# Kernel optimization log

Measured on AMD Instinct MI355X. Metric: run time of the kernel, lower is better.

The kernel has to match this reference:

```python
import jax, jax.numpy as jnp
import numpy as np
from jax import lax


def setup_inputs() -> dict:
    key = jax.random.key(0)
    k1, k2, k3 = jax.random.split(key, 3)
    B, T, D, K = 64, 512, 1024, 32
    x = jax.random.normal(k1, (B, T, D), dtype=jnp.float32)
    W = jax.random.normal(k2, (D, K), dtype=jnp.float32) * (1.0 / np.sqrt(D))
    U = jax.random.normal(k3, (K, K), dtype=jnp.float32) * 0.1
    b = jnp.zeros((K,), dtype=jnp.float32)
    return {"x": x, "W": W, "U": U, "b": b}


def _crf_marginals(x, W, U, b):
    # Emission (input) energies: linear activation of x @ W + b -> [B, T, K]
    e = jnp.einsum('btd,dk->btk', x, W) + b
    e_t = jnp.swapaxes(e, 0, 1)  # [T, B, K]

    # Forward recursion: alpha_t = logsumexp_prev(alpha_{t-1} + U) + e_t
    def fwd_step(alpha, et):
        a = jax.nn.logsumexp(alpha[:, :, None] + U[None, :, :], axis=1) + et
        return a, a

    alpha0 = e_t[0]
    _, alphas = lax.scan(fwd_step, alpha0, e_t[1:])
    alpha = jnp.concatenate([alpha0[None], alphas], axis=0)  # [T, B, K]

    # Backward recursion: beta_t = logsumexp_next(U + e_{t+1} + beta_{t+1})
    def bwd_step(beta, et_next):
        nb = jax.nn.logsumexp(U[None, :, :] + (et_next + beta)[:, None, :], axis=2)
        return nb, nb

    betaT = jnp.zeros_like(alpha0)
    _, betas = lax.scan(bwd_step, betaT, e_t[1:], reverse=True)
    beta = jnp.concatenate([betas, betaT[None]], axis=0)  # [T, B, K]

    # Marginal probability of each tag at each timestep
    marg = jax.nn.softmax(alpha + beta, axis=-1)  # [T, B, K]
    return jnp.swapaxes(marg, 0, 1)  # [B, T, K]


def reference(x, W, U, b):
    return _crf_marginals(x, W, U, b)
```

## Files before the change

kernel.cpp:

```cpp
#include <hip/hip_runtime.h>
#include <stdint.h>

#define TT 512
#define BB 64
#define DD 1024
#define KK 32

typedef __attribute__((ext_vector_type(8))) short short8v;
typedef __attribute__((ext_vector_type(4))) float f4v;

__device__ __forceinline__ float rfl(float v) {
  return __int_as_float(__builtin_amdgcn_readfirstlane(__float_as_int(v)));
}

__device__ __forceinline__ void cvt2(float f0, float f1,
                                     unsigned& h, unsigned& lo) {
  unsigned u0 = __float_as_uint(f0), u1 = __float_as_uint(f1);
  h = (u1 & 0xFFFF0000u) | (u0 >> 16);
  float r0 = f0 - __uint_as_float(u0 & 0xFFFF0000u);
  float r1 = f1 - __uint_as_float(u1 & 0xFFFF0000u);
  lo = (__float_as_uint(r1) & 0xFFFF0000u) | (__float_as_uint(r0) >> 16);
}

__global__ __launch_bounds__(256) void wconv_kernel(
    const float* __restrict__ W, uint4* __restrict__ Wf) {
  const int t = blockIdx.x * 256 + threadIdx.x;
  const int l = t & 63;
  const int kt = (t >> 6) & 1;
  const int c = t >> 7;
  const int d0 = c * 32 + (l >> 4) * 8;
  const int k = kt * 16 + (l & 15);
  unsigned h[4], q[4];
#pragma unroll
  for (int j = 0; j < 4; ++j) {
    float f0 = W[(size_t)(d0 + 2 * j) * KK + k];
    float f1 = W[(size_t)(d0 + 2 * j + 1) * KK + k];
    cvt2(f0, f1, h[j], q[j]);
  }
  Wf[(size_t)(c * 4 + kt * 2 + 0) * 64 + l] = make_uint4(h[0], h[1], h[2], h[3]);
  Wf[(size_t)(c * 4 + kt * 2 + 1) * 64 + l] = make_uint4(q[0], q[1], q[2], q[3]);
}

__global__ __launch_bounds__(256, 4) void emit_kernel(
    const float* __restrict__ x, const uint4* __restrict__ Wf,
    const float* __restrict__ bias, float* __restrict__ F) {
  __shared__ float Ls[4 * 64 * 8];
  const int t = threadIdx.x;
  const int l = t & 63;
  const int w = t >> 6;
  const int rt = w >> 1;
  const int h = w & 1;
  const int m0 = blockIdx.x * 32;
  const int base_r = m0 + rt * 16;

  const float* xp = x + (size_t)(base_r + (l & 15)) * DD + h * 512 + (l >> 4) * 8;
  const uint4* Wp = Wf + l;

  f4v acc0 = {0.f, 0.f, 0.f, 0.f};
  f4v acc1 = {0.f, 0.f, 0.f, 0.f};

  float4 xa[4][2];
  uint4 wv[2][4];
#pragma unroll
  for (int i = 0; i < 4; ++i) {
    xa[i][0] = *(const float4*)(xp + i * 32);
    xa[i][1] = *(const float4*)(xp + i * 32 + 4);
  }
#pragma unroll
  for (int i = 0; i < 2; ++i)
#pragma unroll
    for (int j = 0; j < 4; ++j)
      wv[i][j] = Wp[(size_t)((h * 16 + i) * 4 + j) * 64];

#pragma unroll
  for (int c = 0; c < 16; ++c) {
    const float4 a0 = xa[c & 3][0];
    const float4 a1 = xa[c & 3][1];
    unsigned h0, h1, h2, h3, q0, q1, q2, q3;
    cvt2(a0.x, a0.y, h0, q0); cvt2(a0.z, a0.w, h1, q1);
    cvt2(a1.x, a1.y, h2, q2); cvt2(a1.z, a1.w, h3, q3);
    const uint4 ahu = make_uint4(h0, h1, h2, h3);
    const uint4 alu = make_uint4(q0, q1, q2, q3);
    const short8v Ah = __builtin_bit_cast(short8v, ahu);
    const short8v Al = __builtin_bit_cast(short8v, alu);
    const short8v Bh0 = __builtin_bit_cast(short8v, wv[c & 1][0]);
    const short8v Bl0 = __builtin_bit_cast(short8v, wv[c & 1][1]);
    const short8v Bh1 = __builtin_bit_cast(short8v, wv[c & 1][2]);
    const short8v Bl1 = __builtin_bit_cast(short8v, wv[c & 1][3]);
    if (c + 4 < 16) {
      xa[c & 3][0] = *(const float4*)(xp + (c + 4) * 32);
      xa[c & 3][1] = *(const float4*)(xp + (c + 4) * 32 + 4);
    }
    if (c + 2 < 16) {
#pragma unroll
      for (int j = 0; j < 4; ++j)
        wv[c & 1][j] = Wp[(size_t)((h * 16 + c + 2) * 4 + j) * 64];
    }
    acc0 = __builtin_amdgcn_mfma_f32_16x16x32_bf16(Ah, Bh0, acc0, 0, 0, 0);
    acc1 = __builtin_amdgcn_mfma_f32_16x16x32_bf16(Ah, Bh1, acc1, 0, 0, 0);
    acc0 = __builtin_amdgcn_mfma_f32_16x16x32_bf16(Al, Bh0, acc0, 0, 0, 0);
    acc1 = __builtin_amdgcn_mfma_f32_16x16x32_bf16(Al, Bh1, acc1, 0, 0, 0);
    acc0 = __builtin_amdgcn_mfma_f32_16x16x32_bf16(Ah, Bl0, acc0, 0, 0, 0);
    acc1 = __builtin_amdgcn_mfma_f32_16x16x32_bf16(Ah, Bl1, acc1, 0, 0, 0);
  }

  {
    float* qp = Ls + (w * 64 + l) * 8;
#pragma unroll
    for (int j = 0; j < 4; ++j) { qp[j] = acc0[j]; qp[4 + j] = acc1[j]; }
  }
  __syncthreads();
  if (h == 0) {
    const float* p2 = Ls + ((w + 1) * 64 + l) * 8;
    const int col = l & 15;
    const int rb = base_r + (l >> 4) * 4;
    const float b0 = bias[col];
    const float b1 = bias[col + 16];
#pragma unroll
    for (int j = 0; j < 4; ++j) {
      F[(size_t)(rb + j) * KK + col]      = __expf(acc0[j] + p2[j]     + b0);
      F[(size_t)(rb + j) * KK + col + 16] = __expf(acc1[j] + p2[4 + j] + b1);
    }
  }
}

__global__ __launch_bounds__(64) void scan_kernel(
    const float* __restrict__ F, const float* __restrict__ U,
    float* __restrict__ A, float* __restrict__ Bw) {
  __shared__ __align__(16) float cur[KK];
  const int l = threadIdx.x;
  const int kk = l & 31;
  const int h = l >> 5;
  const int seg = blockIdx.x & 15;
  const int b = (blockIdx.x >> 4) & 63;
  const int dir = blockIdx.x >> 10;

  const float* Fb = F + (size_t)b * TT * KK;
  float V[16];

  if (dir == 0) {
    float* Ab = A + (size_t)b * TT * KK;
#pragma unroll
    for (int j = 0; j < 16; ++j) V[j] = __expf(U[(h * 16 + j) * KK + kk]);
    const int lo = seg * 32, hi = seg * 32 + 31;
    const int t0 = (seg == 0) ? 0 : lo - 17;
    float a = Fb[t0 * KK + kk];
    cur[kk] = a;
    if (seg == 0 && l < 32) Ab[l] = a;
    __builtin_amdgcn_wave_barrier();

#define FSTEP(fv, tcur)                                                     \
    {                                                                       \
      const float4* c4 = (const float4*)cur;                                \
      float4 y0 = c4[h*4+0], y1 = c4[h*4+1], y2 = c4[h*4+2], y3 = c4[h*4+3];\
      float r = __builtin_amdgcn_rcpf(rfl(y0.x));                           \
      float s0 = fmaf(y0.x, V[0],  fmaf(y0.y, V[1],                         \
                 fmaf(y0.z, V[2],  y0.w * V[3])));                          \
      float s1 = fmaf(y1.x, V[4],  fmaf(y1.y, V[5],                         \
                 fmaf(y1.z, V[6],  y1.w * V[7])));                          \
      float s2 = fmaf(y2.x, V[8],  fmaf(y2.y, V[9],                         \
                 fmaf(y2.z, V[10], y2.w * V[11])));                         \
      float s3 = fmaf(y3.x, V[12], fmaf(y3.y, V[13],                        \
                 fmaf(y3.z, V[14], y3.w * V[15])));                         \
      float s = (s0 + s1) + (s2 + s3);                                      \
      s += __shfl_xor(s, 32);                                               \
      a = s * ((fv) * r);                                                   \
      cur[kk] = a;                                                          \
      __builtin_amdgcn_wave_barrier();                                      \
      if ((tcur) >= lo && l < 32) Ab[(tcur) * KK + l] = a;                  \
    }

    int t = t0 + 1;
    float f0 = Fb[t * KK + kk],       f1 = Fb[(t + 1) * KK + kk];
    float f2 = Fb[(t + 2) * KK + kk], f3 = Fb[(t + 3) * KK + kk];
    for (; t + 3 <= hi; t += 4) {
      int tn = t + 4;
      int u0 = tn     > hi ? hi : tn;
      int u1 = tn + 1 > hi ? hi : tn + 1;
      int u2 = tn + 2 > hi ? hi : tn + 2;
      int u3 = tn + 3 > hi ? hi : tn + 3;
      float n0 = Fb[u0 * KK + kk], n1 = Fb[u1 * KK + kk];
      float n2 = Fb[u2 * KK + kk], n3 = Fb[u3 * KK + kk];
      FSTEP(f0, t); FSTEP(f1, t + 1); FSTEP(f2, t + 2); FSTEP(f3, t + 3);
      f0 = n0; f1 = n1; f2 = n2; f3 = n3;
    }
    if (t <= hi) { FSTEP(f0, t); ++t; }
    if (t <= hi) { FSTEP(f1, t); ++t; }
    if (t <= hi) { FSTEP(f2, t); ++t; }
#undef FSTEP
  } else {
    const int b2 = b;
    float* Bb = Bw + (size_t)b2 * TT * KK;
#pragma unroll
    for (int j = 0; j < 16; ++j) V[j] = __expf(U[kk * KK + h * 16 + j]);
    const int lo = seg * 32;
    const int hs = seg * 32 + 31;
    const int t1 = (seg == 15) ? (TT - 1) : (lo + 48);
    float g = Fb[t1 * KK + kk];
    cur[kk] = g;
    if (seg == 15 && l < 32) Bb[(TT - 1) * KK + l] = 1.0f;
    __builtin_amdgcn_wave_barrier();

#define BSTEP(fv, tcur)                                                     \
    {                                                                       \
      const float4* c4 = (const float4*)cur;                                \
      float4 y0 = c4[h*4+0], y1 = c4[h*4+1], y2 = c4[h*4+2], y3 = c4[h*4+3];\
      float r = __builtin_amdgcn_rcpf(rfl(y0.x));                           \
      float s0 = fmaf(y0.x, V[0],  fmaf(y0.y, V[1],                         \
                 fmaf(y0.z, V[2],  y0.w * V[3])));                          \
      float s1 = fmaf(y1.x, V[4],  fmaf(y1.y, V[5],                         \
                 fmaf(y1.z, V[6],  y1.w * V[7])));                          \
      float s2 = fmaf(y2.x, V[8],  fmaf(y2.y, V[9],                         \
                 fmaf(y2.z, V[10], y2.w * V[11])));                         \
      float s3 = fmaf(y3.x, V[12], fmaf(y3.y, V[13],                        \
                 fmaf(y3.z, V[14], y3.w * V[15])));                         \
      float s = (s0 + s1) + (s2 + s3);                                      \
      s += __shfl_xor(s, 32);                                               \
      float bnew = s * r;                                                   \
      g = bnew * (fv);                                                      \
      cur[kk] = g;                                                          \
      __builtin_amdgcn_wave_barrier();                                      \
      if ((tcur) <= hs && l < 32) Bb[(tcur) * KK + l] = bnew;               \
    }

    int t = t1 - 1;
    float f0 = Fb[t * KK + kk],       f1 = Fb[(t - 1) * KK + kk];
    float f2 = Fb[(t - 2) * KK + kk], f3 = Fb[(t - 3) * KK + kk];
    for (; t - 3 >= lo; t -= 4) {
      int tn = t - 4;
      int u0 = tn     < 0 ? 0 : tn;
      int u1 = tn - 1 < 0 ? 0 : tn - 1;
      int u2 = tn - 2 < 0 ? 0 : tn - 2;
      int u3 = tn - 3 < 0 ? 0 : tn - 3;
      float n0 = Fb[u0 * KK + kk], n1 = Fb[u1 * KK + kk];
      float n2 = Fb[u2 * KK + kk], n3 = Fb[u3 * KK + kk];
      BSTEP(f0, t); BSTEP(f1, t - 1); BSTEP(f2, t - 2); BSTEP(f3, t - 3);
      f0 = n0; f1 = n1; f2 = n2; f3 = n3;
    }
    if (t >= lo) { BSTEP(f0, t); --t; }
    if (t >= lo) { BSTEP(f1, t); --t; }
    if (t >= lo) { BSTEP(f2, t); --t; }
#undef BSTEP
  }
}

__global__ __launch_bounds__(256) void combine_kernel(
    const float* __restrict__ Bw, float* __restrict__ out) {
  size_t i = (size_t)blockIdx.x * 256 + threadIdx.x;
  float p = out[i] * Bw[i];
  float ssum = p;
  ssum += __shfl_xor(ssum, 1);
  ssum += __shfl_xor(ssum, 2);
  ssum += __shfl_xor(ssum, 4);
  ssum += __shfl_xor(ssum, 8);
  ssum += __shfl_xor(ssum, 16);
  out[i] = p / ssum;
}

extern "C" void kernel_launch(void* const* d_in, const int* in_sizes, int n_in,
                              void* d_out, int out_size, void* d_ws, size_t ws_size,
                              hipStream_t stream) {
  const float* x = (const float*)d_in[0];
  const float* W = (const float*)d_in[1];
  const float* U = (const float*)d_in[2];
  const float* b = (const float*)d_in[3];
  float* out = (float*)d_out;
  float* F = (float*)d_ws;
  float* Bw = F + (size_t)BB * TT * KK;
  uint4* Wf = (uint4*)(Bw + (size_t)BB * TT * KK);

  wconv_kernel<<<16, 256, 0, stream>>>(W, Wf);
  emit_kernel<<<1024, 256, 0, stream>>>(x, Wf, b, F);
  scan_kernel<<<2048, 64, 0, stream>>>(F, U, out, Bw);
  combine_kernel<<<(BB * TT * KK) / 256, 256, 0, stream>>>(Bw, out);
}
```

Measured before the change: 218.5 us.

## Stage x tiles into LDS via direct global-to-LDS loads with XOR swizzle

The emission GEMM now loads a whole 16-row x tile (64 KB) into LDS using global_load_lds 16-byte transfers with an XOR swizzle, rather than having each wave stream x into registers. The work is split as 16 rows per block with four waves each covering a quarter of D, and a four-way reduction through LDS. The grid doubles to 2048 blocks. The aim is fully coalesced row reads and less register pressure on the x stream. The cost is 64 KB of LDS per block, which limits occupancy, and a barrier before any compute, so loads no longer overlap with MFMA work inside a block.

```diff
diff --git a/kernel.cpp b/kernel.cpp
--- a/kernel.cpp
+++ b/kernel.cpp
@@ -11,6 +11,12 @@
 
 __device__ __forceinline__ float rfl(float v) {
   return __int_as_float(__builtin_amdgcn_readfirstlane(__float_as_int(v)));
+}
+
+__device__ __forceinline__ void gload_lds16(const float4* g, float4* l) {
+  __builtin_amdgcn_global_load_lds(
+      (const __attribute__((address_space(1))) uint32_t*)g,
+      (__attribute__((address_space(3))) uint32_t*)l, 16, 0, 0);
 }
 
 __device__ __forceinline__ void cvt2(float f0, float f1,
@@ -41,41 +47,45 @@
   Wf[(size_t)(c * 4 + kt * 2 + 1) * 64 + l] = make_uint4(q[0], q[1], q[2], q[3]);
 }
 
-__global__ __launch_bounds__(256, 4) void emit_kernel(
+__global__ __launch_bounds__(256) void emit_kernel(
     const float* __restrict__ x, const uint4* __restrict__ Wf,
     const float* __restrict__ bias, float* __restrict__ F) {
-  __shared__ float Ls[4 * 64 * 8];
+  __shared__ float4 Lx4[16 * 256];
   const int t = threadIdx.x;
   const int l = t & 63;
   const int w = t >> 6;
-  const int rt = w >> 1;
-  const int h = w & 1;
-  const int m0 = blockIdx.x * 32;
-  const int base_r = m0 + rt * 16;
-
-  const float* xp = x + (size_t)(base_r + (l & 15)) * DD + h * 512 + (l >> 4) * 8;
+  const int m0 = blockIdx.x * 16;
+
+  {
+    const float* xb = x + (size_t)m0 * DD;
+#pragma unroll
+    for (int i = 0; i < 16; ++i) {
+      const int row = 4 * w + (i >> 2);
+      const int qd = i & 3;
+      const float* src =
+          xb + (size_t)row * DD + qd * 256 + (l ^ (row & 7)) * 4;
+      gload_lds16((const float4*)src, &Lx4[row * 256 + qd * 64]);
+    }
+  }
+  __syncthreads();
+
+  const int r_ = l & 15, dg_ = l >> 4;
   const uint4* Wp = Wf + l;
-
   f4v acc0 = {0.f, 0.f, 0.f, 0.f};
   f4v acc1 = {0.f, 0.f, 0.f, 0.f};
 
-  float4 xa[4][2];
   uint4 wv[2][4];
 #pragma unroll
-  for (int i = 0; i < 4; ++i) {
-    xa[i][0] = *(const float4*)(xp + i * 32);
-    xa[i][1] = *(const float4*)(xp + i * 32 + 4);
-  }
-#pragma unroll
   for (int i = 0; i < 2; ++i)
 #pragma unroll
     for (int j = 0; j < 4; ++j)
-      wv[i][j] = Wp[(size_t)((h * 16 + i) * 4 + j) * 64];
-
-#pragma unroll
-  for (int c = 0; c < 16; ++c) {
-    const float4 a0 = xa[c & 3][0];
-    const float4 a1 = xa[c & 3][1];
+      wv[i][j] = Wp[(size_t)((w * 8 + i) * 4 + j) * 64];
+
+  const int abase = r_ * 256 + w * 64;
+#pragma unroll
+  for (int ks = 0; ks < 8; ++ks) {
+    float4 a0 = Lx4[abase + ((ks * 8 + dg_ * 2 + 0) ^ (r_ & 7))];
+    float4 a1 = Lx4[abase + ((ks * 8 + dg_ * 2 + 1) ^ (r_ & 7))];
     unsigned h0, h1, h2, h3, q0, q1, q2, q3;
     cvt2(a0.x, a0.y, h0, q0); cvt2(a0.z, a0.w, h1, q1);
     cvt2(a1.x, a1.y, h2, q2); cvt2(a1.z, a1.w, h3, q3);
@@ -83,18 +93,14 @@
     const uint4 alu = make_uint4(q0, q1, q2, q3);
     const short8v Ah = __builtin_bit_cast(short8v, ahu);
     const short8v Al = __builtin_bit_cast(short8v, alu);
-    const short8v Bh0 = __builtin_bit_cast(short8v, wv[c & 1][0]);
-    const short8v Bl0 = __builtin_bit_cast(short8v, wv[c & 1][1]);
-    const short8v Bh1 = __builtin_bit_cast(short8v, wv[c & 1][2]);
-    const short8v Bl1 = __builtin_bit_cast(short8v, wv[c & 1][3]);
-    if (c + 4 < 16) {
-      xa[c & 3][0] = *(const float4*)(xp + (c + 4) * 32);
-      xa[c & 3][1] = *(const float4*)(xp + (c + 4) * 32 + 4);
-    }
-    if (c + 2 < 16) {
+    const short8v Bh0 = __builtin_bit_cast(short8v, wv[ks & 1][0]);
+    const short8v Bl0 = __builtin_bit_cast(short8v, wv[ks & 1][1]);
+    const short8v Bh1 = __builtin_bit_cast(short8v, wv[ks & 1][2]);
+    const short8v Bl1 = __builtin_bit_cast(short8v, wv[ks & 1][3]);
+    if (ks + 2 < 8) {
 #pragma unroll
       for (int j = 0; j < 4; ++j)
-        wv[c & 1][j] = Wp[(size_t)((h * 16 + c + 2) * 4 + j) * 64];
+        wv[ks & 1][j] = Wp[(size_t)((w * 8 + ks + 2) * 4 + j) * 64];
     }
     acc0 = __builtin_amdgcn_mfma_f32_16x16x32_bf16(Ah, Bh0, acc0, 0, 0, 0);
     acc1 = __builtin_amdgcn_mfma_f32_16x16x32_bf16(Ah, Bh1, acc1, 0, 0, 0);
@@ -104,22 +110,33 @@
     acc1 = __builtin_amdgcn_mfma_f32_16x16x32_bf16(Ah, Bl1, acc1, 0, 0, 0);
   }
 
+  __syncthreads();
   {
+    float* Ls = (float*)Lx4;
     float* qp = Ls + (w * 64 + l) * 8;
 #pragma unroll
     for (int j = 0; j < 4; ++j) { qp[j] = acc0[j]; qp[4 + j] = acc1[j]; }
   }
   __syncthreads();
-  if (h == 0) {
-    const float* p2 = Ls + ((w + 1) * 64 + l) * 8;
+  if (w == 0) {
+    const float* Ls = (const float*)Lx4;
+    float s0[4], s1[4];
+#pragma unroll
+    for (int j = 0; j < 4; ++j) { s0[j] = acc0[j]; s1[j] = acc1[j]; }
+#pragma unroll
+    for (int q = 1; q < 4; ++q) {
+      const float* p2 = Ls + ((q * 64 + l) * 8);
+#pragma unroll
+      for (int j = 0; j < 4; ++j) { s0[j] += p2[j]; s1[j] += p2[4 + j]; }
+    }
     const int col = l & 15;
-    const int rb = base_r + (l >> 4) * 4;
+    const int rb = m0 + (l >> 4) * 4;
     const float b0 = bias[col];
     const float b1 = bias[col + 16];
 #pragma unroll
     for (int j = 0; j < 4; ++j) {
-      F[(size_t)(rb + j) * KK + col]      = __expf(acc0[j] + p2[j]     + b0);
-      F[(size_t)(rb + j) * KK + col + 16] = __expf(acc1[j] + p2[4 + j] + b1);
+      F[(size_t)(rb + j) * KK + col]      = __expf(s0[j] + b0);
+      F[(size_t)(rb + j) * KK + col + 16] = __expf(s1[j] + b1);
     }
   }
 }
@@ -270,7 +287,7 @@
   uint4* Wf = (uint4*)(Bw + (size_t)BB * TT * KK);
 
   wconv_kernel<<<16, 256, 0, stream>>>(W, Wf);
-  emit_kernel<<<1024, 256, 0, stream>>>(x, Wf, b, F);
+  emit_kernel<<<2048, 256, 0, stream>>>(x, Wf, b, F);
   scan_kernel<<<2048, 64, 0, stream>>>(F, U, out, Bw);
   combine_kernel<<<(BB * TT * KK) / 256, 256, 0, stream>>>(Bw, out);
 }
```

New measurement: 214.4 us. No clear change (-1.9%).
